# Optimization experiments

Hardware: AMD Instinct MI355X
Metric: run time of the kernel (lower is better)

The kernel has to match this reference:

```python
import jax, jax.numpy as jnp
import numpy as np
from jax import lax

C = 192       # filter_channels
L = 3         # n_layers
K = 3         # kernel_size
NB = 10       # num_bins
TB = 5.0      # tail_bound
HALF = 1      # in_channels // 2


def setup_inputs() -> dict:
    key = jax.random.key(0)
    ks = jax.random.split(key, 8)
    s = lambda i, shape: jax.random.normal(ks[i], shape, jnp.float32) * 0.05
    return {
        "x": jax.random.normal(ks[0], (16, 2, 8192), jnp.float32),
        "x_mask": jnp.ones((16, 1, 8192), jnp.float32),
        "w_pre": s(1, (C, HALF)), "b_pre": jnp.zeros((C,), jnp.float32),
        "sep_w": s(2, (L, K, 1, C)), "sep_b": jnp.zeros((L, C), jnp.float32),
        "pw_w": s(3, (L, C, C)), "pw_b": jnp.zeros((L, C), jnp.float32),
        "n1_g": jnp.ones((L, C), jnp.float32), "n1_b": jnp.zeros((L, C), jnp.float32),
        "n2_g": jnp.ones((L, C), jnp.float32), "n2_b": jnp.zeros((L, C), jnp.float32),
        "w_proj": s(4, (HALF * (3 * NB - 1), C)),
        "b_proj": jnp.zeros((HALF * (3 * NB - 1),), jnp.float32),
    }


def _layernorm_c(x, g, b, eps=1e-5):
    # normalize over channel axis (axis=1) of [b, c, t]
    m = jnp.mean(x, axis=1, keepdims=True)
    v = jnp.var(x, axis=1, keepdims=True)
    return (x - m) * lax.rsqrt(v + eps) * g[:, None] + b[:, None]


def _rq_spline(x, uw, uh, ud, tail_bound=TB, mw=1e-3, mh=1e-3, md=1e-3):
    """Unconstrained rational-quadratic spline with linear tails (forward)."""
    nb = uw.shape[-1]
    inside = (x >= -tail_bound) & (x <= tail_bound)
    const = float(np.log(np.exp(1.0 - md) - 1.0))
    ud = jnp.pad(ud, [(0, 0)] * (ud.ndim - 1) + [(1, 1)], constant_values=const)

    widths = jax.nn.softmax(uw, axis=-1)
    widths = mw + (1.0 - mw * nb) * widths
    cw = jnp.pad(jnp.cumsum(widths, -1), [(0, 0)] * (widths.ndim - 1) + [(1, 0)])
    cw = -tail_bound + 2.0 * tail_bound * cw
    cw = cw.at[..., 0].set(-tail_bound).at[..., -1].set(tail_bound)
    w = cw[..., 1:] - cw[..., :-1]

    heights = jax.nn.softmax(uh, axis=-1)
    heights = mh + (1.0 - mh * nb) * heights
    ch = jnp.pad(jnp.cumsum(heights, -1), [(0, 0)] * (heights.ndim - 1) + [(1, 0)])
    ch = -tail_bound + 2.0 * tail_bound * ch
    ch = ch.at[..., 0].set(-tail_bound).at[..., -1].set(tail_bound)
    hgt = ch[..., 1:] - ch[..., :-1]

    d = md + jax.nn.softplus(ud)  # [..., nb+1]

    xi = jnp.clip(x, -tail_bound, tail_bound)
    # searchsorted-style bin lookup
    idx = jnp.clip(jnp.sum((xi[..., None] >= cw).astype(jnp.int32), -1) - 1, 0, nb - 1)
    take = lambda p: jnp.take_along_axis(p, idx[..., None], axis=-1)[..., 0]

    in_cw, in_w = take(cw), take(w)
    in_ch, in_h = take(ch), take(hgt)
    in_d, d_p = take(d), take(d[..., 1:])
    delta = in_h / in_w

    th = (xi - in_cw) / in_w
    th1 = th * (1.0 - th)
    num = in_h * (delta * th * th + in_d * th1)
    den = delta + (in_d + d_p - 2.0 * delta) * th1
    y = in_ch + num / den
    dnum = delta * delta * (d_p * th * th + 2.0 * delta * th1 + in_d * (1.0 - th) ** 2)
    lad = jnp.log(dnum) - 2.0 * jnp.log(den)

    y = jnp.where(inside, y, x)
    lad = jnp.where(inside, lad, jnp.zeros_like(lad))
    return y, lad


def reference(x, x_mask, w_pre, b_pre, sep_w, sep_b, pw_w, pw_b,
              n1_g, n1_b, n2_g, n2_b, w_proj, b_proj):
    x0, x1 = x[:, :HALF], x[:, HALF:]

    # pre: 1x1 conv
    h = jnp.einsum('bct,fc->bft', x0, w_pre) + b_pre[:, None]

    # DDSConv: depthwise dilated conv + 1x1 + LayerNorm + GELU, residual
    for i in range(L):
        y = lax.conv_general_dilated(
            h * x_mask, sep_w[i], window_strides=(1,), padding='SAME',
            rhs_dilation=(K ** i,),
            dimension_numbers=('NCH', 'HIO', 'NCH'),
            feature_group_count=C) + sep_b[i][:, None]
        y = jax.nn.gelu(_layernorm_c(y, n1_g[i], n1_b[i]), approximate=False)
        y = jnp.einsum('bct,oc->bot', y, pw_w[i]) + pw_b[i][:, None]
        y = jax.nn.gelu(_layernorm_c(y, n2_g[i], n2_b[i]), approximate=False)
        h = h + y
    h = h * x_mask

    # proj: 1x1 conv to spline params
    h = (jnp.einsum('bct,oc->bot', h, w_proj) + b_proj[:, None]) * x_mask

    b, c, t = x0.shape
    h = h.reshape(b, c, 3 * NB - 1, t).transpose(0, 1, 3, 2)  # [b, c, t, 3*NB-1]
    scale = 1.0 / np.sqrt(C).astype(np.float32)
    uw = h[..., :NB] * scale
    uh = h[..., NB:2 * NB] * scale
    ud = h[..., 2 * NB:]

    y1, lad = _rq_spline(x1, uw, uh, ud)
    out = jnp.concatenate([x0, y1], axis=1) * x_mask
    logdet = jnp.sum(lad * x_mask, axis=(1, 2))
    return out, logdet
```

## Files before the change

### kernel.cpp

```cpp
#include <hip/hip_runtime.h>

#define CC    192
#define EXT   64
#define LDC   200
#define NTH   512
#define HALO  13
#define INTR  38
#define TT    8192
#define BATCH 16
#define NTILES 216
#define NPROJ 29

#define WQ1_ELEMS (3*6*12*512)
#define WQ2_ELEMS (6*2*512)

typedef __bf16 bf16x8 __attribute__((ext_vector_type(8)));
typedef __bf16 bf16x4 __attribute__((ext_vector_type(4)));
typedef __bf16 bf16x2 __attribute__((ext_vector_type(2)));
typedef float  f32x4  __attribute__((ext_vector_type(4)));

__device__ __forceinline__ float gelu_fast(float v) {
    float vv = v * v;
    float u2 = v * fmaf(0.0713548162f, vv, 1.5957691216f);
    float t  = __expf(u2);
    float r  = __builtin_amdgcn_rcpf(t + 1.0f);
    return v - v * r;
}
__device__ __forceinline__ float softplus_f(float v) {
    float e = __expf(-fabsf(v));
    return fmaxf(v, 0.0f) + __logf(1.0f + e);
}

__global__ __launch_bounds__(256) void prepack_kernel(
    const float* __restrict__ pw_w, const float* __restrict__ w_proj,
    __bf16* __restrict__ wq, __bf16* __restrict__ wq2) {
    int idx = blockIdx.x * 256 + threadIdx.x;
    if (idx < WQ1_ELEMS) {
        int e    = idx & 7;
        int lane = (idx >> 3) & 63;
        int r    = idx >> 9;
        int mt   = r % 12;
        int ks   = (r / 12) % 6;
        int li   = r / 72;
        int o = 16 * mt + (lane & 15);
        int c = 32 * ks + 8 * (lane >> 4) + e;
        wq[idx] = (__bf16)pw_w[((size_t)li * CC + o) * CC + c];
    } else if (idx < WQ1_ELEMS + WQ2_ELEMS) {
        int i2   = idx - WQ1_ELEMS;
        int e    = i2 & 7;
        int lane = (i2 >> 3) & 63;
        int r    = i2 >> 9;
        int pr   = r % 2;
        int ks   = r / 2;
        int row  = 16 * pr + (lane & 15);
        int c    = 32 * ks + 8 * (lane >> 4) + e;
        wq2[i2] = (row < NPROJ) ? (__bf16)w_proj[(size_t)row * CC + c] : (__bf16)0.0f;
    }
}

__global__ __launch_bounds__(NTH, 4) void convflow_kernel(
    const float* __restrict__ x, const float* __restrict__ xmask,
    const float* __restrict__ w_pre, const float* __restrict__ b_pre,
    const float* __restrict__ sep_w, const float* __restrict__ sep_b,
    const __bf16* __restrict__ wq, const __bf16* __restrict__ wq2,
    const float* __restrict__ pw_b,
    const float* __restrict__ n1_g, const float* __restrict__ n1_b,
    const float* __restrict__ n2_g, const float* __restrict__ n2_b,
    const float* __restrict__ b_proj,
    float* __restrict__ out, float* __restrict__ logdet)
{
    extern __shared__ char smemraw[];
    __bf16* __restrict__ sh_t = (__bf16*)smemraw;
    __bf16* __restrict__ syt  = sh_t + EXT * LDC;
    float*  __restrict__ sproj = (float*)syt;
    __bf16* __restrict__ spb  = syt + EXT * LDC;
    __bf16* __restrict__ sg2  = spb + CC;
    __bf16* __restrict__ sb2  = sg2 + CC;

#define SXROW(j) ((float*)(smemraw + (size_t)(j)*400 + 384))
#define SREDP(j) ((float2*)(smemraw + 25600 + (size_t)(j)*400 + 384))

    const int tid  = threadIdx.x;
    const int lane = tid & 63;
    const int wav  = tid >> 6;
    const int b    = blockIdx.x / NTILES;
    const int tile = blockIdx.x - b * NTILES;
    const int t0   = tile * INTR - HALO;

    for (int j = tid; j < EXT; j += NTH) {
        int t = t0 + j;
        bool ok = (t >= 0) && (t < TT);
        float* sxr = SXROW(j);
        sxr[0] = ok ? x[b*2*TT + t]      : 0.0f;
        sxr[1] = ok ? x[b*2*TT + TT + t] : 0.0f;
        sxr[2] = ok ? xmask[b*TT + t]    : 0.0f;
    }
    __syncthreads();

    for (int e = tid; e < CC*EXT; e += NTH) {
        int c = e % CC;
        int j = e / CC;
        const float* sxr = SXROW(j);
        sh_t[j*LDC + c] = (__bf16)((sxr[0] * w_pre[c] + b_pre[c]) * sxr[2]);
    }
    for (int q = tid; q < INTR; q += NTH) {
        int t = t0 + HALO + q;
        const float* sxr = SXROW(HALO+q);
        if (t < TT) out[b*2*TT + t] = sxr[0] * sxr[2];
    }
    __syncthreads();

    const int g   = lane >> 4;
    const int c15 = lane & 15;
    const int cl  = lane & 31;
    const int sub = lane >> 5;
    const int nt   = wav & 3;
    const int half = wav >> 2;

    #pragma unroll
    for (int li = 0; li < 3; ++li) {
        constexpr int DILA[3] = {1, 3, 9};
        constexpr int JLOA[3] = {1, 4, 13};
        constexpr int JHIA[3] = {63, 60, 51};
        const int dil = DILA[li];
        const int jlo = JLOA[li], jhi = JHIA[li];

        for (int i = tid; i < CC; i += NTH) {
            spb[i] = (__bf16)pw_b[li*CC + i];
            sg2[i] = (__bf16)n2_g[li*CC + i];
            sb2[i] = (__bf16)n2_b[li*CC + i];
        }

        {
            float k0[6], k1[6], k2[6], cb[6], g1[6], b1[6];
            #pragma unroll
            for (int k = 0; k < 6; ++k) {
                int c = 6*cl + k;
                k0[k] = sep_w[(li*3+0)*CC + c];
                k1[k] = sep_w[(li*3+1)*CC + c];
                k2[k] = sep_w[(li*3+2)*CC + c];
                cb[k] = sep_b[li*CC + c];
                g1[k] = n1_g[li*CC + c];
                b1[k] = n1_b[li*CC + c];
            }
            for (int j = jlo + 2*wav + sub; j < jhi; j += 16) {
                float m0 = SXROW(j-dil)[2], m1 = SXROW(j)[2], m2 = SXROW(j+dil)[2];
                (void)m0; (void)m1; (void)m2;
                const bf16x2* r0 = (const bf16x2*)(sh_t + (j-dil)*LDC + 6*cl);
                const bf16x2* r1 = (const bf16x2*)(sh_t + j*LDC       + 6*cl);
                const bf16x2* r2 = (const bf16x2*)(sh_t + (j+dil)*LDC + 6*cl);
                bf16x2 t0v[3], t1v[3], t2v[3];
                #pragma unroll
                for (int p = 0; p < 3; ++p) { t0v[p] = r0[p]; t1v[p] = r1[p]; t2v[p] = r2[p]; }
                float a[6]; float s = 0.0f, ss = 0.0f;
                #pragma unroll
                for (int k = 0; k < 6; ++k) {
                    float v = k0[k]*(float)t0v[k>>1][k&1]
                            + k1[k]*(float)t1v[k>>1][k&1]
                            + k2[k]*(float)t2v[k>>1][k&1] + cb[k];
                    a[k] = v; s += v; ss += v*v;
                }
                #pragma unroll
                for (int mm = 1; mm < 32; mm <<= 1) {
                    s  += __shfl_xor(s,  mm, 64);
                    ss += __shfl_xor(ss, mm, 64);
                }
                float mean = s * (1.0f/CC);
                float var  = ss * (1.0f/CC) - mean*mean;
                float rstd = rsqrtf(var + 1e-5f);
                #pragma unroll
                for (int p = 0; p < 3; ++p) {
                    bf16x2 w;
                    w[0] = (__bf16)gelu_fast((a[2*p+0]-mean)*rstd*g1[2*p+0] + b1[2*p+0]);
                    w[1] = (__bf16)gelu_fast((a[2*p+1]-mean)*rstd*g1[2*p+1] + b1[2*p+1]);
                    *(bf16x2*)(syt + j*LDC + 6*cl + 2*p) = w;
                }
            }
        }
        __syncthreads();

        {
            f32x4 acc[6];
            #pragma unroll
            for (int q = 0; q < 6; ++q) {
                bf16x4 pb = *(const bf16x4*)(spb + 16*(6*half+q) + 4*g);
                acc[q][0] = (float)pb[0]; acc[q][1] = (float)pb[1];
                acc[q][2] = (float)pb[2]; acc[q][3] = (float)pb[3];
            }
            const __bf16* wql = wq + (size_t)li * (6*12*512);
            #pragma unroll
            for (int ks = 0; ks < 6; ++ks) {
                bf16x8 bfrag = *(const bf16x8*)(syt + (16*nt + c15)*LDC + 32*ks + 8*g);
                const __bf16* ap = wql + (size_t)(ks*12 + 6*half)*512 + lane*8;
                #pragma unroll
                for (int q = 0; q < 6; ++q) {
                    bf16x8 afrag = *(const bf16x8*)(ap + (size_t)q*512);
                    acc[q] = __builtin_amdgcn_mfma_f32_16x16x32_bf16(afrag, bfrag, acc[q], 0, 0, 0);
                }
            }
            float s = 0.0f, ss = 0.0f;
            #pragma unroll
            for (int q = 0; q < 6; ++q) {
                #pragma unroll
                for (int e = 0; e < 4; ++e) { float z = acc[q][e]; s += z; ss += z*z; }
            }
            s  += __shfl_xor(s, 16, 64);  s  += __shfl_xor(s, 32, 64);
            ss += __shfl_xor(ss, 16, 64); ss += __shfl_xor(ss, 32, 64);
            if (lane < 16) SREDP(16*nt + lane)[half] = make_float2(s, ss);
            __syncthreads();
            const int col = 16*nt + c15;
            float2 e0 = SREDP(col)[0], e1 = SREDP(col)[1];
            float mean = (e0.x + e1.x) * (1.0f/CC);
            float var  = (e0.y + e1.y) * (1.0f/CC) - mean*mean;
            float rstd = rsqrtf(var + 1e-5f);
            float mj   = SXROW(col)[2];
            #pragma unroll
            for (int q = 0; q < 6; ++q) {
                int mt = 6*half + q;
                bf16x4 gv = *(const bf16x4*)(sg2 + 16*mt + 4*g);
                bf16x4 bv = *(const bf16x4*)(sb2 + 16*mt + 4*g);
                bf16x4 hv = *(bf16x4*)(sh_t + (size_t)col*LDC + 16*mt + 4*g);
                hv[0] = (__bf16)((float)hv[0] + gelu_fast((acc[q][0]-mean)*rstd*(float)gv[0] + (float)bv[0])*mj);
                hv[1] = (__bf16)((float)hv[1] + gelu_fast((acc[q][1]-mean)*rstd*(float)gv[1] + (float)bv[1])*mj);
                hv[2] = (__bf16)((float)hv[2] + gelu_fast((acc[q][2]-mean)*rstd*(float)gv[2] + (float)bv[2])*mj);
                hv[3] = (__bf16)((float)hv[3] + gelu_fast((acc[q][3]-mean)*rstd*(float)gv[3] + (float)bv[3])*mj);
                *(bf16x4*)(sh_t + (size_t)col*LDC + 16*mt + 4*g) = hv;
            }
        }
        __syncthreads();
    }

    {
        const int pr = half;
        f32x4 p0 = {0,0,0,0};
        #pragma unroll
        for (int ks = 0; ks < 6; ++ks) {
            bf16x8 bfrag = *(const bf16x8*)(sh_t + (16*nt + c15)*LDC + 32*ks + 8*g);
            bf16x8 a0 = *(const bf16x8*)(wq2 + (size_t)(ks*2 + pr)*512 + lane*8);
            p0 = __builtin_amdgcn_mfma_f32_16x16x32_bf16(a0, bfrag, p0, 0, 0, 0);
        }
        const int col = 16*nt + c15;
        if (col >= HALO && col < HALO + INTR) {
            float mj = SXROW(col)[2];
            #pragma unroll
            for (int e = 0; e < 4; ++e) {
                int p = 16*pr + 4*g + e;
                if (p < NPROJ) sproj[col*33 + p] = (p0[e] + b_proj[p])*mj;
            }
        }
    }
    __syncthreads();

    if (tid < 64) {
        int j = HALO + tid;
        int t = t0 + j;
        float ladm = 0.0f;
        if (tid < INTR && t < TT) {
            const float SCALE = 0.07216878364870323f;
            float mj = SXROW(j)[2];
            float xv = SXROW(j)[1];
            float uw[10], uh[10];
            #pragma unroll
            for (int k = 0; k < 10; ++k) {
                uw[k] = sproj[j*33 + k]      * SCALE;
                uh[k] = sproj[j*33 + 10 + k] * SCALE;
            }
            float mxw = uw[0];
            #pragma unroll
            for (int k = 1; k < 10; ++k) mxw = fmaxf(mxw, uw[k]);
            float ew[10]; float sew = 0.0f;
            #pragma unroll
            for (int k = 0; k < 10; ++k) { ew[k] = __expf(uw[k]-mxw); sew += ew[k]; }
            float invw = 1.0f/sew;
            float cw[11]; cw[0] = -5.0f;
            float run = 0.0f;
            #pragma unroll
            for (int k = 0; k < 10; ++k) { run += 0.001f + 0.99f*ew[k]*invw; cw[k+1] = -5.0f + 10.0f*run; }
            cw[10] = 5.0f;
            float mxh = uh[0];
            #pragma unroll
            for (int k = 1; k < 10; ++k) mxh = fmaxf(mxh, uh[k]);
            float eh[10]; float seh = 0.0f;
            #pragma unroll
            for (int k = 0; k < 10; ++k) { eh[k] = __expf(uh[k]-mxh); seh += eh[k]; }
            float invh = 1.0f/seh;
            float ch[11]; ch[0] = -5.0f;
            run = 0.0f;
            #pragma unroll
            for (int k = 0; k < 10; ++k) { run += 0.001f + 0.99f*eh[k]*invh; ch[k+1] = -5.0f + 10.0f*run; }
            ch[10] = 5.0f;
            float dd[11];
            dd[0] = 1.0f;
            #pragma unroll
            for (int k = 0; k < 9; ++k) dd[k+1] = 0.001f + softplus_f(sproj[j*33 + 20 + k]);
            dd[10] = 1.0f;

            bool inside = (xv >= -5.0f) && (xv <= 5.0f);
            float xi = fminf(fmaxf(xv, -5.0f), 5.0f);
            int idx = 0;
            #pragma unroll
            for (int k = 1; k <= 9; ++k) idx = (xi >= cw[k]) ? k : idx;
            float in_cw=0, in_w=1, in_ch=0, in_h=1, in_d=1, d_p=1;
            #pragma unroll
            for (int k = 0; k < 10; ++k) {
                if (k == idx) {
                    in_cw = cw[k]; in_w = cw[k+1]-cw[k];
                    in_ch = ch[k]; in_h = ch[k+1]-ch[k];
                    in_d  = dd[k]; d_p  = dd[k+1];
                }
            }
            float delta = in_h/in_w;
            float th  = (xi - in_cw)/in_w;
            float th1 = th*(1.0f-th);
            float num = in_h*(delta*th*th + in_d*th1);
            float den = delta + (in_d + d_p - 2.0f*delta)*th1;
            float yv  = in_ch + num/den;
            float omt = 1.0f - th;
            float dnum = delta*delta*(d_p*th*th + 2.0f*delta*th1 + in_d*omt*omt);
            float lad = __logf(dnum) - 2.0f*__logf(den);
            if (!inside) { yv = xv; lad = 0.0f; }
            out[b*2*TT + TT + t] = yv*mj;
            ladm = lad*mj;
        }
        #pragma unroll
        for (int mm = 1; mm < 64; mm <<= 1) ladm += __shfl_xor(ladm, mm, 64);
        if (tid == 0) atomicAdd(&logdet[b], ladm);
    }
#undef SXROW
#undef SREDP
}

extern "C" void kernel_launch(void* const* d_in, const int* in_sizes, int n_in,
                              void* d_out, int out_size, void* d_ws, size_t ws_size,
                              hipStream_t stream) {
    const float* x      = (const float*)d_in[0];
    const float* xmask  = (const float*)d_in[1];
    const float* w_pre  = (const float*)d_in[2];
    const float* b_pre  = (const float*)d_in[3];
    const float* sep_w  = (const float*)d_in[4];
    const float* sep_b  = (const float*)d_in[5];
    const float* pw_w   = (const float*)d_in[6];
    const float* pw_b   = (const float*)d_in[7];
    const float* n1_g   = (const float*)d_in[8];
    const float* n1_b   = (const float*)d_in[9];
    const float* n2_g   = (const float*)d_in[10];
    const float* n2_b   = (const float*)d_in[11];
    const float* w_proj = (const float*)d_in[12];
    const float* b_proj = (const float*)d_in[13];
    float* out = (float*)d_out;
    float* logdet = out + (size_t)BATCH*2*TT;
    __bf16* wq  = (__bf16*)d_ws;
    __bf16* wq2 = wq + WQ1_ELEMS;

    hipMemsetAsync((void*)logdet, 0, BATCH*sizeof(float), stream);
    prepack_kernel<<<dim3((WQ1_ELEMS + WQ2_ELEMS + 255)/256), 256, 0, stream>>>(
        pw_w, w_proj, wq, wq2);

    size_t shbytes = (size_t)(2*EXT*LDC*2 + 3*CC*2);
    dim3 grid(BATCH*NTILES);
    convflow_kernel<<<grid, NTH, shbytes, stream>>>(
        x, xmask, w_pre, b_pre, sep_w, sep_b, wq, wq2, pw_b,
        n1_g, n1_b, n2_g, n2_b, b_proj, out, logdet);
}
```

Baseline: 256.8 us.

## Enlarge time tiles to 80 columns with 10 waves to cut halo overhead

Grows each block's extended time window from 64 to 80 columns, so each tile keeps 54 interior samples instead of 38. The block goes from 8 to 10 waves, with the MFMA column tiles remapped to 5 per half, and the tile count per batch drops to 152. This cuts the share of halo recomputation, at the cost of more LDS and threads per block, which can lower occupancy. It also stores pw_b and the second LayerNorm gamma/beta as fp32 in LDS instead of bf16, rewrites the GELU exponent to use exp2 with prescaled constants, and drops unused mask loads.

```diff
diff --git a/kernel.cpp b/kernel.cpp
--- a/kernel.cpp
+++ b/kernel.cpp
@@ -1,14 +1,14 @@
 #include <hip/hip_runtime.h>
 
 #define CC    192
-#define EXT   64
+#define EXT   80
 #define LDC   200
-#define NTH   512
+#define NTH   640
 #define HALO  13
-#define INTR  38
+#define INTR  54
 #define TT    8192
 #define BATCH 16
-#define NTILES 216
+#define NTILES 152
 #define NPROJ 29
 
 #define WQ1_ELEMS (3*6*12*512)
@@ -21,8 +21,8 @@
 
 __device__ __forceinline__ float gelu_fast(float v) {
     float vv = v * v;
-    float u2 = v * fmaf(0.0713548162f, vv, 1.5957691216f);
-    float t  = __expf(u2);
+    float u2 = v * fmaf(0.1029427551f, vv, 2.3022077198f);
+    float t  = exp2f(u2);
     float r  = __builtin_amdgcn_rcpf(t + 1.0f);
     return v - v * r;
 }
@@ -73,12 +73,12 @@
     __bf16* __restrict__ sh_t = (__bf16*)smemraw;
     __bf16* __restrict__ syt  = sh_t + EXT * LDC;
     float*  __restrict__ sproj = (float*)syt;
-    __bf16* __restrict__ spb  = syt + EXT * LDC;
-    __bf16* __restrict__ sg2  = spb + CC;
-    __bf16* __restrict__ sb2  = sg2 + CC;
+    float*  __restrict__ spb  = (float*)(syt + EXT * LDC);
+    float*  __restrict__ sg2  = spb + CC;
+    float*  __restrict__ sb2  = sg2 + CC;
 
 #define SXROW(j) ((float*)(smemraw + (size_t)(j)*400 + 384))
-#define SREDP(j) ((float2*)(smemraw + 25600 + (size_t)(j)*400 + 384))
+#define SREDP(j) ((float2*)(smemraw + 32000 + (size_t)(j)*400 + 384))
 
     const int tid  = threadIdx.x;
     const int lane = tid & 63;
@@ -114,21 +114,21 @@
     const int c15 = lane & 15;
     const int cl  = lane & 31;
     const int sub = lane >> 5;
-    const int nt   = wav & 3;
-    const int half = wav >> 2;
+    const int half = (wav >= 5) ? 1 : 0;
+    const int nt   = wav - 5*half;
 
     #pragma unroll
     for (int li = 0; li < 3; ++li) {
         constexpr int DILA[3] = {1, 3, 9};
         constexpr int JLOA[3] = {1, 4, 13};
-        constexpr int JHIA[3] = {63, 60, 51};
+        constexpr int JHIA[3] = {79, 76, 67};
         const int dil = DILA[li];
         const int jlo = JLOA[li], jhi = JHIA[li];
 
         for (int i = tid; i < CC; i += NTH) {
-            spb[i] = (__bf16)pw_b[li*CC + i];
-            sg2[i] = (__bf16)n2_g[li*CC + i];
-            sb2[i] = (__bf16)n2_b[li*CC + i];
+            spb[i] = pw_b[li*CC + i];
+            sg2[i] = n2_g[li*CC + i];
+            sb2[i] = n2_b[li*CC + i];
         }
 
         {
@@ -143,9 +143,7 @@
                 g1[k] = n1_g[li*CC + c];
                 b1[k] = n1_b[li*CC + c];
             }
-            for (int j = jlo + 2*wav + sub; j < jhi; j += 16) {
-                float m0 = SXROW(j-dil)[2], m1 = SXROW(j)[2], m2 = SXROW(j+dil)[2];
-                (void)m0; (void)m1; (void)m2;
+            for (int j = jlo + 2*wav + sub; j < jhi; j += 20) {
                 const bf16x2* r0 = (const bf16x2*)(sh_t + (j-dil)*LDC + 6*cl);
                 const bf16x2* r1 = (const bf16x2*)(sh_t + j*LDC       + 6*cl);
                 const bf16x2* r2 = (const bf16x2*)(sh_t + (j+dil)*LDC + 6*cl);
@@ -183,9 +181,8 @@
             f32x4 acc[6];
             #pragma unroll
             for (int q = 0; q < 6; ++q) {
-                bf16x4 pb = *(const bf16x4*)(spb + 16*(6*half+q) + 4*g);
-                acc[q][0] = (float)pb[0]; acc[q][1] = (float)pb[1];
-                acc[q][2] = (float)pb[2]; acc[q][3] = (float)pb[3];
+                float4 pb = *(const float4*)(spb + 16*(6*half+q) + 4*g);
+                acc[q][0] = pb.x; acc[q][1] = pb.y; acc[q][2] = pb.z; acc[q][3] = pb.w;
             }
             const __bf16* wql = wq + (size_t)li * (6*12*512);
             #pragma unroll
@@ -217,13 +214,13 @@
             #pragma unroll
             for (int q = 0; q < 6; ++q) {
                 int mt = 6*half + q;
-                bf16x4 gv = *(const bf16x4*)(sg2 + 16*mt + 4*g);
-                bf16x4 bv = *(const bf16x4*)(sb2 + 16*mt + 4*g);
+                float4 gv = *(const float4*)(sg2 + 16*mt + 4*g);
+                float4 bv = *(const float4*)(sb2 + 16*mt + 4*g);
                 bf16x4 hv = *(bf16x4*)(sh_t + (size_t)col*LDC + 16*mt + 4*g);
-                hv[0] = (__bf16)((float)hv[0] + gelu_fast((acc[q][0]-mean)*rstd*(float)gv[0] + (float)bv[0])*mj);
-                hv[1] = (__bf16)((float)hv[1] + gelu_fast((acc[q][1]-mean)*rstd*(float)gv[1] + (float)bv[1])*mj);
-                hv[2] = (__bf16)((float)hv[2] + gelu_fast((acc[q][2]-mean)*rstd*(float)gv[2] + (float)bv[2])*mj);
-                hv[3] = (__bf16)((float)hv[3] + gelu_fast((acc[q][3]-mean)*rstd*(float)gv[3] + (float)bv[3])*mj);
+                hv[0] = (__bf16)((float)hv[0] + gelu_fast((acc[q][0]-mean)*rstd*gv.x + bv.x)*mj);
+                hv[1] = (__bf16)((float)hv[1] + gelu_fast((acc[q][1]-mean)*rstd*gv.y + bv.y)*mj);
+                hv[2] = (__bf16)((float)hv[2] + gelu_fast((acc[q][2]-mean)*rstd*gv.z + bv.z)*mj);
+                hv[3] = (__bf16)((float)hv[3] + gelu_fast((acc[q][3]-mean)*rstd*gv.w + bv.w)*mj);
                 *(bf16x4*)(sh_t + (size_t)col*LDC + 16*mt + 4*g) = hv;
             }
         }
@@ -356,7 +353,7 @@
     prepack_kernel<<<dim3((WQ1_ELEMS + WQ2_ELEMS + 255)/256), 256, 0, stream>>>(
         pw_w, w_proj, wq, wq2);
 
-    size_t shbytes = (size_t)(2*EXT*LDC*2 + 3*CC*2);
+    size_t shbytes = (size_t)(2*EXT*LDC*2 + 3*CC*4);
     dim3 grid(BATCH*NTILES);
     convflow_kernel<<<grid, NTH, shbytes, stream>>>(
         x, xmask, w_pre, b_pre, sep_w, sep_b, wq, wq2, pw_b,
```

After: 331.6 us. 29.2% more time.
